# Kernel optimization log

Measured on AMD Instinct MI355X. Metric: run time of the kernel, lower is better.

Reference implementation:

```python
import jax, jax.numpy as jnp
import numpy as np

BN_EPS = 1e-5

def conv1x1(x, w, b):
    # x: [B,C,H,W], w: [O,C], b: [O]
    return jnp.einsum('bchw,oc->bohw', x, w) + b[None, :, None, None]

def bn_inf(x, gamma, beta, mean, var):
    inv = gamma / jnp.sqrt(var + BN_EPS)
    return (x - mean[None, :, None, None]) * inv[None, :, None, None] + beta[None, :, None, None]

def setup_inputs() -> dict:
    key = jax.random.key(0)
    ks = jax.random.split(key, 24)
    B, Fg, Fl, Fi = 8, 256, 256, 64
    H = W = 64
    c8 = Fi // 8
    d = {}
    d['g'] = jax.random.normal(ks[0], (B, Fg, H, W), jnp.float32)
    d['x'] = jax.random.normal(ks[1], (B, Fl, H, W), jnp.float32)
    # W_g: conv1x1 + BN
    d['Wg_w'] = jax.random.normal(ks[2], (Fi, Fg), jnp.float32) * (1.0 / np.sqrt(Fg))
    d['Wg_b'] = jax.random.normal(ks[3], (Fi,), jnp.float32) * 0.02
    d['bng_gamma'] = jax.random.uniform(ks[4], (Fi,), jnp.float32, 0.5, 1.5)
    d['bng_beta'] = jax.random.normal(ks[5], (Fi,), jnp.float32) * 0.1
    d['bng_mean'] = jax.random.normal(ks[6], (Fi,), jnp.float32) * 0.1
    d['bng_var'] = jax.random.uniform(ks[7], (Fi,), jnp.float32, 0.5, 1.5)
    # W_x: conv1x1 + BN
    d['Wx_w'] = jax.random.normal(ks[8], (Fi, Fl), jnp.float32) * (1.0 / np.sqrt(Fl))
    d['Wx_b'] = jax.random.normal(ks[9], (Fi,), jnp.float32) * 0.02
    d['bnx_gamma'] = jax.random.uniform(ks[10], (Fi,), jnp.float32, 0.5, 1.5)
    d['bnx_beta'] = jax.random.normal(ks[11], (Fi,), jnp.float32) * 0.1
    d['bnx_mean'] = jax.random.normal(ks[12], (Fi,), jnp.float32) * 0.1
    d['bnx_var'] = jax.random.uniform(ks[13], (Fi,), jnp.float32, 0.5, 1.5)
    # psi: conv1x1 (Fi->1) + BN(1) + sigmoid
    d['psi_w'] = jax.random.normal(ks[14], (1, Fi), jnp.float32) * (1.0 / np.sqrt(Fi))
    d['psi_b'] = jax.random.normal(ks[15], (1,), jnp.float32) * 0.02
    d['bnp_gamma'] = jax.random.uniform(ks[16], (1,), jnp.float32, 0.5, 1.5)
    d['bnp_beta'] = jax.random.normal(ks[17], (1,), jnp.float32) * 0.1
    d['bnp_mean'] = jax.random.normal(ks[18], (1,), jnp.float32) * 0.1
    d['bnp_var'] = jax.random.uniform(ks[19], (1,), jnp.float32, 0.5, 1.5)
    # PAM convs
    d['pb_w'] = jax.random.normal(ks[20], (c8, Fi), jnp.float32) * (1.0 / np.sqrt(Fi))
    d['pb_b'] = jnp.zeros((c8,), jnp.float32)
    d['pc_w'] = jax.random.normal(ks[21], (c8, Fi), jnp.float32) * (1.0 / np.sqrt(Fi))
    d['pc_b'] = jnp.zeros((c8,), jnp.float32)
    d['pd_w'] = jax.random.normal(ks[22], (Fi, Fi), jnp.float32) * (1.0 / np.sqrt(Fi))
    d['pd_b'] = jnp.zeros((Fi,), jnp.float32)
    # scalar gates (torch inits to 0; use small nonzero to exercise the path)
    d['alpha'] = jax.random.normal(ks[23], (1,), jnp.float32) * 0.05
    d['cam_beta'] = jax.random.normal(jax.random.fold_in(key, 99), (1,), jnp.float32) * 0.05
    return d

def _cam(psi, cam_beta):
    B, C, H, W = psi.shape
    feat = psi.reshape(B, C, H * W)                       # [B,C,HW]
    att = jnp.einsum('bcn,bdn->bcd', feat, feat)          # [B,C,C]
    att_new = jnp.max(att, axis=-1, keepdims=True) - att  # max-subtract trick
    att = jax.nn.softmax(att_new, axis=-1)
    out = jnp.einsum('bcd,bdn->bcn', att, feat).reshape(B, C, H, W)
    return cam_beta[0] * out + psi

def _pam(psi, pb_w, pb_b, pc_w, pc_b, pd_w, pd_b, alpha):
    B, C, H, W = psi.shape
    HW = H * W
    fb = conv1x1(psi, pb_w, pb_b).reshape(B, -1, HW)      # [B,C/8,HW]
    fc = conv1x1(psi, pc_w, pc_b).reshape(B, -1, HW)      # [B,C/8,HW]
    energy = jnp.einsum('bki,bkj->bij', fb, fc)           # [B,HW,HW]
    att = jax.nn.softmax(energy, axis=-1)
    fd = conv1x1(psi, pd_w, pd_b).reshape(B, C, HW)       # [B,C,HW]
    out = jnp.einsum('bcj,bij->bci', fd, att).reshape(B, C, H, W)
    return alpha[0] * out + psi

def reference(g, x, Wg_w, Wg_b, bng_gamma, bng_beta, bng_mean, bng_var,
              Wx_w, Wx_b, bnx_gamma, bnx_beta, bnx_mean, bnx_var,
              psi_w, psi_b, bnp_gamma, bnp_beta, bnp_mean, bnp_var,
              pb_w, pb_b, pc_w, pc_b, pd_w, pd_b, alpha, cam_beta):
    g1 = bn_inf(conv1x1(g, Wg_w, Wg_b), bng_gamma, bng_beta, bng_mean, bng_var)
    x1 = bn_inf(conv1x1(x, Wx_w, Wx_b), bnx_gamma, bnx_beta, bnx_mean, bnx_var)
    psi = jax.nn.relu(g1 + x1)                            # [B,F_int,H,W]
    cam = _cam(psi, cam_beta)
    pam = _pam(psi, pb_w, pb_b, pc_w, pc_b, pd_w, pd_b, alpha)
    gate = bn_inf(conv1x1(cam * pam, psi_w, psi_b), bnp_gamma, bnp_beta, bnp_mean, bnp_var)
    da = jax.nn.sigmoid(gate)                             # [B,1,H,W]
    return x * da
```

## Files before the change

### kernel.cpp

```cpp
#include <hip/hip_runtime.h>
#include <hip/hip_bf16.h>
#include <math.h>

#define BB 8
#define CIN 256
#define FI 64
#define HW 4096
#define C8 8
#define EPS 1e-5f
#define LOG2E 1.4426950408889634f

typedef __attribute__((ext_vector_type(8))) short bf16x8;
typedef __attribute__((ext_vector_type(4))) float f32x4;
typedef unsigned short u16;

static __device__ __forceinline__ u16 f2b(float x) {
    unsigned u = __builtin_bit_cast(unsigned, x);
    return (u16)((u + 0x8000u) >> 16);
}
static __device__ __forceinline__ unsigned cvtpk(float a, float b) {
    unsigned r;
    asm("v_cvt_pk_bf16_f32 %0, %1, %2" : "=v"(r) : "v"(a), "v"(b));
    return r;
}
static __device__ __forceinline__ float b2f(u16 v) {
    return __builtin_bit_cast(float, ((unsigned)v) << 16);
}

__global__ __launch_bounds__(256) void k_prep(
    const float* __restrict__ Wg, const float* __restrict__ Wgb,
    const float* __restrict__ gg, const float* __restrict__ gbeta,
    const float* __restrict__ gm, const float* __restrict__ gv,
    const float* __restrict__ Wx, const float* __restrict__ Wxb,
    const float* __restrict__ xg, const float* __restrict__ xbeta,
    const float* __restrict__ xm, const float* __restrict__ xv,
    const float* __restrict__ pbw, const float* __restrict__ pbb,
    const float* __restrict__ pcw, const float* __restrict__ pcb,
    const float* __restrict__ pdw, const float* __restrict__ pdb,
    u16* __restrict__ Wp, float* __restrict__ Cp,
    u16* __restrict__ Wcat, float* __restrict__ bcat)
{
    const int gid = blockIdx.x * 256 + threadIdx.x;
    for (int idx = gid; idx < FI * 512; idx += 4096) {
        int o = idx >> 9, k = idx & 511;
        float s, w;
        if (k < 256) { s = gg[o] * rsqrtf(gv[o] + EPS); w = Wg[o * 256 + k]; }
        else         { s = xg[o] * rsqrtf(xv[o] + EPS); w = Wx[o * 256 + k - 256]; }
        Wp[idx] = f2b(w * s);
    }
    for (int idx = gid; idx < 80 * 64; idx += 4096) {
        int row = idx >> 6, col = idx & 63;
        float w;
        if (row < 8)       w = pbw[row * 64 + col] * LOG2E;
        else if (row < 16) w = pcw[(row - 8) * 64 + col];
        else               w = pdw[(row - 16) * 64 + col];
        Wcat[idx] = f2b(w);
    }
    if (blockIdx.x == 0) {
        int tid = threadIdx.x;
        if (tid < FI) {
            float ig = gg[tid] * rsqrtf(gv[tid] + EPS);
            float ix = xg[tid] * rsqrtf(xv[tid] + EPS);
            Cp[tid] = (Wgb[tid] - gm[tid]) * ig + gbeta[tid]
                    + (Wxb[tid] - xm[tid]) * ix + xbeta[tid];
        }
        if (tid >= 64 && tid < 144) {
            int r = tid - 64;
            float bv = (r < 8) ? pbb[r] * LOG2E : (r < 16 ? pcb[r - 8] : pdb[r - 16]);
            bcat[r] = bv;
        }
    }
}

__global__ __launch_bounds__(256) void k_psi(
    const float* __restrict__ g, const float* __restrict__ x,
    const u16* __restrict__ Wp, const float* __restrict__ Cp,
    const u16* __restrict__ Wcat, const float* __restrict__ bcat,
    u16* __restrict__ psiB, u16* __restrict__ psiLo,
    u16* __restrict__ fbcT, u16* __restrict__ fdB)
{
    const int tid  = threadIdx.x;
    const int lane = tid & 63;
    const int w    = tid >> 6;
    const int n    = lane & 15;
    const int quad = lane >> 4;
    const int b    = blockIdx.y;
    const int p0   = blockIdx.x * 64;

    __shared__ u16 InT[64][72];
    __shared__ u16 Tbc[64][16];

    f32x4 acc[4];
#pragma unroll
    for (int mt = 0; mt < 4; ++mt) acc[mt] = (f32x4){0.f, 0.f, 0.f, 0.f};

    for (int kc = 0; kc < 8; ++kc) {
        const float* src = (kc < 4) ? g : x;
        const int ch0 = (kc & 3) * 64;
        __syncthreads();
#pragma unroll
        for (int r = 0; r < 4; ++r) {
            int ch = (tid >> 4) + r * 16;
            int px = (tid & 15) * 4;
            float4 v = *(const float4*)&src[((size_t)b * CIN + ch0 + ch) * HW + p0 + px];
            InT[px][ch]     = f2b(v.x);
            InT[px + 1][ch] = f2b(v.y);
            InT[px + 2][ch] = f2b(v.z);
            InT[px + 3][ch] = f2b(v.w);
        }
        __syncthreads();
#pragma unroll
        for (int ks = 0; ks < 2; ++ks) {
            const int kglob = kc * 64 + ks * 32;
            bf16x8 bfrag = *(const bf16x8*)&InT[w * 16 + n][ks * 32 + quad * 8];
#pragma unroll
            for (int mt = 0; mt < 4; ++mt) {
                bf16x8 af = *(const bf16x8*)&Wp[(mt * 16 + n) * 512 + kglob + quad * 8];
                acc[mt] = __builtin_amdgcn_mfma_f32_16x16x32_bf16(
                              af, bfrag, acc[mt], 0, 0, 0);
            }
        }
    }

    float pv[4][4];
#pragma unroll
    for (int mt = 0; mt < 4; ++mt)
#pragma unroll
        for (int r = 0; r < 4; ++r) {
            int c = mt * 16 + quad * 4 + r;
            float v = acc[mt][r] + Cp[c];
            v = v > 0.f ? v : 0.f;
            pv[mt][r] = v;
            u16 hb = f2b(v);
            size_t idx = ((size_t)b * FI + c) * HW + p0 + w * 16 + n;
            psiB[idx]  = hb;
            psiLo[idx] = f2b(v - b2f(hb));
        }
    __syncthreads();
#pragma unroll
    for (int mt = 0; mt < 4; ++mt) {
        *(unsigned*)&InT[w * 16 + n][mt * 16 + quad * 4]     = cvtpk(pv[mt][0], pv[mt][1]);
        *(unsigned*)&InT[w * 16 + n][mt * 16 + quad * 4 + 2] = cvtpk(pv[mt][2], pv[mt][3]);
    }
    __syncthreads();

    f32x4 facc[5];
#pragma unroll
    for (int nt = 0; nt < 5; ++nt) facc[nt] = (f32x4){0.f, 0.f, 0.f, 0.f};
#pragma unroll
    for (int ks = 0; ks < 2; ++ks) {
        bf16x8 af = *(const bf16x8*)&InT[w * 16 + n][ks * 32 + quad * 8];
#pragma unroll
        for (int nt = 0; nt < 5; ++nt) {
            bf16x8 bf = *(const bf16x8*)&Wcat[(nt * 16 + n) * FI + ks * 32 + quad * 8];
            facc[nt] = __builtin_amdgcn_mfma_f32_16x16x32_bf16(af, bf, facc[nt], 0, 0, 0);
        }
    }
    __syncthreads();

    {
        float bias = bcat[n];
#pragma unroll
        for (int r = 0; r < 4; ++r)
            Tbc[w * 16 + quad * 4 + r][n] = f2b(facc[0][r] + bias);
    }
#pragma unroll
    for (int nt = 1; nt < 5; ++nt) {
        int ch = (nt - 1) * 16 + n;
        float bias = bcat[nt * 16 + n];
        *(unsigned*)&InT[ch][w * 16 + quad * 4]     = cvtpk(facc[nt][0] + bias, facc[nt][1] + bias);
        *(unsigned*)&InT[ch][w * 16 + quad * 4 + 2] = cvtpk(facc[nt][2] + bias, facc[nt][3] + bias);
    }
    __syncthreads();
    {
        int row = tid >> 2, part = tid & 3;
        uint2 v = *(const uint2*)&Tbc[row][part * 4];
        *(uint2*)&fbcT[((size_t)b * HW + p0 + row) * 16 + part * 4] = v;
    }
#pragma unroll
    for (int rep = 0; rep < 2; ++rep) {
        int t = rep * 256 + tid;
        int ch = t >> 3, seg = t & 7;
        bf16x8 v = *(const bf16x8*)&InT[ch][seg * 8];
        *(bf16x8*)&fdB[((size_t)b * FI + ch) * HW + p0 + seg * 8] = v;
    }
}

__global__ __launch_bounds__(256) void k_gram(
    const u16* __restrict__ psiB, const u16* __restrict__ psiLo,
    float* __restrict__ Gp)
{
    const int tid  = threadIdx.x;
    const int lane = tid & 63;
    const int w    = tid >> 6;
    const int n    = lane & 15;
    const int quad = lane >> 4;
    const int s    = blockIdx.x;
    const int b    = blockIdx.y;

    f32x4 acc[4];
#pragma unroll
    for (int nt = 0; nt < 4; ++nt) acc[nt] = (f32x4){0.f, 0.f, 0.f, 0.f};

    for (int ks = 0; ks < 4; ++ks) {
        const int k0 = s * 128 + ks * 32;
        const size_t ra = ((size_t)b * FI + w * 16 + n) * HW + k0 + quad * 8;
        bf16x8 ah = *(const bf16x8*)&psiB[ra];
        bf16x8 al = *(const bf16x8*)&psiLo[ra];
#pragma unroll
        for (int nt = 0; nt < 4; ++nt) {
            const size_t rb = ((size_t)b * FI + nt * 16 + n) * HW + k0 + quad * 8;
            bf16x8 bh = *(const bf16x8*)&psiB[rb];
            bf16x8 bl = *(const bf16x8*)&psiLo[rb];
            acc[nt] = __builtin_amdgcn_mfma_f32_16x16x32_bf16(ah, bh, acc[nt], 0, 0, 0);
            acc[nt] = __builtin_amdgcn_mfma_f32_16x16x32_bf16(ah, bl, acc[nt], 0, 0, 0);
            acc[nt] = __builtin_amdgcn_mfma_f32_16x16x32_bf16(al, bh, acc[nt], 0, 0, 0);
        }
    }
#pragma unroll
    for (int nt = 0; nt < 4; ++nt)
#pragma unroll
        for (int r = 0; r < 4; ++r) {
            int i = w * 16 + quad * 4 + r;
            Gp[(((size_t)s * 8 + b) * 64 + i) * 64 + nt * 16 + n] = acc[nt][r];
        }
}

__global__ __launch_bounds__(256) void k_camsm(
    const float* __restrict__ Gp, float* __restrict__ att)
{
    const int tid = threadIdx.x, d = tid & 63, ty = tid >> 6;
    const int b = blockIdx.x, grp = blockIdx.y;
#pragma unroll 1
    for (int rr = 0; rr < 4; ++rr) {
        int i = grp * 16 + ty * 4 + rr;
        float gsum = 0.f;
#pragma unroll 1
        for (int s = 0; s < 32; ++s) gsum += Gp[(((size_t)s * 8 + b) * 64 + i) * 64 + d];
        float M = gsum;
#pragma unroll
        for (int msk = 1; msk < 64; msk <<= 1) M = fmaxf(M, __shfl_xor(M, msk));
        float a = M - gsum;
        float m2 = a;
#pragma unroll
        for (int msk = 1; msk < 64; msk <<= 1) m2 = fmaxf(m2, __shfl_xor(m2, msk));
        float p = __expf(a - m2);
        float ssum = p;
#pragma unroll
        for (int msk = 1; msk < 64; msk <<= 1) ssum += __shfl_xor(ssum, msk);
        att[((size_t)b * 64 + i) * 64 + d] = p / ssum;
    }
}

__global__ __launch_bounds__(256) void k_pam(
    const u16* __restrict__ fbcT, const u16* __restrict__ fdB,
    u16* __restrict__ Opart, float* __restrict__ ml)
{
    const int tid  = threadIdx.x;
    const int lane = tid & 63;
    const int w    = tid >> 6;
    const int n    = lane & 15;
    const int quad = lane >> 4;
    const int b    = blockIdx.x;
    const int i0   = blockIdx.y * 64;
    const int p    = blockIdx.z;
    const int jstart = p * 32, jend = jstart + 32;

    __shared__ u16 Ks[2][68][8];
    __shared__ u16 Vs[2][64][64];
    __shared__ u16 Ps[4][16][64];

    if (tid < 16) {
        ((unsigned*)&Ks[0][64][0])[tid] = 0u;
        ((unsigned*)&Ks[1][64][0])[tid] = 0u;
    }

    bf16x8 qfrag = {};
    if (quad == 0)
        qfrag = *(const bf16x8*)&fbcT[((size_t)b * HW + i0 + w * 16 + n) * 16];

    const int kkey = tid >> 1, khalf = tid & 1;
    const int vch  = tid >> 3, vseg  = tid & 7;
    const int vslot = (vseg ^ (vch & 7)) << 3;
    const int pswz  = n & 7;

    const u16* kp = fbcT + ((size_t)b * HW + jstart * 64) * 16 + 8;
    const u16* vp = fdB + (size_t)b * FI * HW + jstart * 64;

    uint2 kreg = make_uint2(0u, 0u);
    bf16x8 vreg0, vreg1;
    if (tid < 128) kreg = *(const uint2*)(kp + (size_t)kkey * 16 + khalf * 4);
    vreg0 = *(const bf16x8*)(vp + (size_t)vch * HW + vseg * 8);
    vreg1 = *(const bf16x8*)(vp + (size_t)(32 + vch) * HW + vseg * 8);

    f32x4 oacc[4];
#pragma unroll
    for (int mt = 0; mt < 4; ++mt) oacc[mt] = (f32x4){0.f, 0.f, 0.f, 0.f};
    float m = -1e30f, l = 0.f;

    int cur = 0;
    for (int jc = jstart; jc < jend; ++jc) {
        if (tid < 128) *(uint2*)&Ks[cur][kkey][khalf * 4] = kreg;
        *(bf16x8*)&Vs[cur][vch][vslot]      = vreg0;
        *(bf16x8*)&Vs[cur][32 + vch][vslot] = vreg1;
        if (jc + 1 < jend) {
            kp += 64 * 16;
            vp += 64;
            if (tid < 128) kreg = *(const uint2*)(kp + (size_t)kkey * 16 + khalf * 4);
            vreg0 = *(const bf16x8*)(vp + (size_t)vch * HW + vseg * 8);
            vreg1 = *(const bf16x8*)(vp + (size_t)(32 + vch) * HW + vseg * 8);
        }
        __syncthreads();

        f32x4 s[4];
        __builtin_amdgcn_s_setprio(1);
#pragma unroll
        for (int mt = 0; mt < 4; ++mt) {
            bf16x8 af = *(const bf16x8*)&Ks[cur][mt * 16 + n + quad][0];
            s[mt] = __builtin_amdgcn_mfma_f32_16x16x32_bf16(
                        af, qfrag, (f32x4){0.f, 0.f, 0.f, 0.f}, 0, 0, 0);
        }
        __builtin_amdgcn_s_setprio(0);

        float cmax = -1e30f;
#pragma unroll
        for (int mt = 0; mt < 4; ++mt)
            cmax = fmaxf(cmax, fmaxf(fmaxf(s[mt][0], s[mt][1]),
                                     fmaxf(s[mt][2], s[mt][3])));
        cmax = fmaxf(cmax, __shfl_xor(cmax, 16));
        cmax = fmaxf(cmax, __shfl_xor(cmax, 32));

        if (__any(cmax > m + 8.f)) {
            float mnew  = fmaxf(m, cmax);
            float scale = __builtin_amdgcn_exp2f(m - mnew);
            l *= scale;
#pragma unroll
            for (int mt = 0; mt < 4; ++mt) {
                oacc[mt][0] *= scale; oacc[mt][1] *= scale;
                oacc[mt][2] *= scale; oacc[mt][3] *= scale;
            }
            m = mnew;
        }

        float psum = 0.f;
        unsigned pw[4][2];
#pragma unroll
        for (int mt = 0; mt < 4; ++mt) {
            float e0 = __builtin_amdgcn_exp2f(s[mt][0] - m);
            float e1 = __builtin_amdgcn_exp2f(s[mt][1] - m);
            float e2 = __builtin_amdgcn_exp2f(s[mt][2] - m);
            float e3 = __builtin_amdgcn_exp2f(s[mt][3] - m);
            psum += (e0 + e1) + (e2 + e3);
            pw[mt][0] = cvtpk(e0, e1);
            pw[mt][1] = cvtpk(e2, e3);
        }
        l += psum;

#pragma unroll
        for (int mt = 0; mt < 4; ++mt) {
            int so = (((mt * 2 + (quad >> 1)) ^ pswz) << 3) + ((quad & 1) << 2);
            *(uint2*)&Ps[w][n][so] = make_uint2(pw[mt][0], pw[mt][1]);
        }
        asm volatile("s_waitcnt lgkmcnt(0)" ::: "memory");
        __builtin_amdgcn_sched_barrier(0);

        __builtin_amdgcn_s_setprio(1);
#pragma unroll
        for (int k0 = 0; k0 < 2; ++k0) {
            bf16x8 pf = *(const bf16x8*)&Ps[w][n][((k0 * 4 + quad) ^ pswz) << 3];
#pragma unroll
            for (int mt = 0; mt < 4; ++mt) {
                bf16x8 vf = *(const bf16x8*)
                    &Vs[cur][mt * 16 + n][((k0 * 4 + quad) ^ pswz) << 3];
                oacc[mt] = __builtin_amdgcn_mfma_f32_16x16x32_bf16(
                               vf, pf, oacc[mt], 0, 0, 0);
            }
        }
        __builtin_amdgcn_s_setprio(0);
        cur ^= 1;
    }

    l += __shfl_xor(l, 16);
    l += __shfl_xor(l, 32);
    const float rl = 1.f / l;
#pragma unroll
    for (int mt = 0; mt < 4; ++mt)
#pragma unroll
        for (int r = 0; r < 4; ++r) {
            int c = mt * 16 + quad * 4 + r;
            Opart[(((size_t)p * 8 + b) * FI + c) * HW + i0 + w * 16 + n] =
                f2b(oacc[mt][r] * rl);
        }
    if (quad == 0)
        ((float2*)ml)[((size_t)p * 8 + b) * HW + i0 + w * 16 + n] = make_float2(m, l);
}

__global__ __launch_bounds__(256) void k_final(
    const u16* __restrict__ psiB, const u16* __restrict__ psiLo,
    const float* __restrict__ att,
    const u16* __restrict__ Opart, const float* __restrict__ ml,
    const float* __restrict__ x,
    const float* __restrict__ psiw, const float* __restrict__ psib,
    const float* __restrict__ pg, const float* __restrict__ pbeta,
    const float* __restrict__ pm, const float* __restrict__ pv,
    const float* __restrict__ alpha, const float* __restrict__ camb,
    float* __restrict__ out)
{
    const int tid = threadIdx.x, tx = tid & 63, ty = tid >> 6;
    const int b = blockIdx.y, p0 = blockIdx.x * 64;
    __shared__ float tp[64][65];
    __shared__ float A[64][64];
    __shared__ float Zp[4][64];

#pragma unroll
    for (int r = 0; r < 16; ++r) {
        int c = ty * 16 + r;
        size_t idx = ((size_t)b * FI + c) * HW + p0 + tx;
        tp[c][tx] = b2f(psiB[idx]) + b2f(psiLo[idx]);
        A[c][tx]  = att[((size_t)b * 64 + c) * 64 + tx];
    }
    __syncthreads();

    float2 ml0 = ((const float2*)ml)[((size_t)0 * 8 + b) * HW + p0 + tx];
    float2 ml1 = ((const float2*)ml)[((size_t)1 * 8 + b) * HW + p0 + tx];
    float M  = fmaxf(ml0.x, ml1.x);
    float w0 = ml0.y * __builtin_amdgcn_exp2f(ml0.x - M);
    float w1 = ml1.y * __builtin_amdgcn_exp2f(ml1.x - M);
    float winv = 1.f / (w0 + w1);
    w0 *= winv; w1 *= winv;

    const float al = alpha[0], cb = camb[0];
    const int c0 = __builtin_amdgcn_readfirstlane(ty * 16);
    float acc[16];
#pragma unroll
    for (int i = 0; i < 16; ++i) acc[i] = 0.f;
#pragma unroll 16
    for (int d = 0; d < 64; ++d) {
        float v = tp[d][tx];
#pragma unroll
        for (int i = 0; i < 16; ++i) acc[i] += A[c0 + i][d] * v;
    }
    float z = 0.f;
#pragma unroll
    for (int i = 0; i < 16; ++i) {
        int c = c0 + i;
        float ps  = tp[c][tx];
        float cam = cb * acc[i] + ps;
        float oa = w0 * b2f(Opart[(((size_t)0 * 8 + b) * FI + c) * HW + p0 + tx])
                 + w1 * b2f(Opart[(((size_t)1 * 8 + b) * FI + c) * HW + p0 + tx]);
        float pam = al * oa + ps;
        z += psiw[c] * (cam * pam);
    }
    Zp[ty][tx] = z;
    __syncthreads();
    float zt = Zp[0][tx] + Zp[1][tx] + Zp[2][tx] + Zp[3][tx] + psib[0];
    float inv = pg[0] * rsqrtf(pv[0] + EPS);
    float gate = (zt - pm[0]) * inv + pbeta[0];
    float da = 1.f / (1.f + __expf(-gate));

#pragma unroll 8
    for (int r = 0; r < 64; ++r) {
        int cl = ty + 4 * r;
        size_t idx = ((size_t)b * CIN + cl) * HW + p0 + tx;
        out[idx] = x[idx] * da;
    }
}

extern "C" void kernel_launch(void* const* d_in, const int* in_sizes, int n_in,
                              void* d_out, int out_size, void* d_ws, size_t ws_size,
                              hipStream_t stream)
{
    const float* g     = (const float*)d_in[0];
    const float* x     = (const float*)d_in[1];
    const float* Wg_w  = (const float*)d_in[2];
    const float* Wg_b  = (const float*)d_in[3];
    const float* bng_g = (const float*)d_in[4];
    const float* bng_b = (const float*)d_in[5];
    const float* bng_m = (const float*)d_in[6];
    const float* bng_v = (const float*)d_in[7];
    const float* Wx_w  = (const float*)d_in[8];
    const float* Wx_b  = (const float*)d_in[9];
    const float* bnx_g = (const float*)d_in[10];
    const float* bnx_b = (const float*)d_in[11];
    const float* bnx_m = (const float*)d_in[12];
    const float* bnx_v = (const float*)d_in[13];
    const float* psi_w = (const float*)d_in[14];
    const float* psi_b = (const float*)d_in[15];
    const float* bnp_g = (const float*)d_in[16];
    const float* bnp_b = (const float*)d_in[17];
    const float* bnp_m = (const float*)d_in[18];
    const float* bnp_v = (const float*)d_in[19];
    const float* pb_w  = (const float*)d_in[20];
    const float* pb_b  = (const float*)d_in[21];
    const float* pc_w  = (const float*)d_in[22];
    const float* pc_b  = (const float*)d_in[23];
    const float* pd_w  = (const float*)d_in[24];
    const float* pd_b  = (const float*)d_in[25];
    const float* alpha = (const float*)d_in[26];
    const float* camb  = (const float*)d_in[27];
    float* out = (float*)d_out;

    float* ws   = (float*)d_ws;
    u16*  psiB  = (u16*)(ws);
    u16*  psiLo = (u16*)(ws + 1048576);
    u16*  fbcT  = (u16*)(ws + 2097152);
    u16*  fdB   = (u16*)(ws + 2359296);
    float* att  = ws + 3407872;
    u16*  Wp    = (u16*)(ws + 3440640);
    float* Cp   = ws + 3457024;
    u16*  Wcat  = (u16*)(ws + 3457088);
    float* bcat = ws + 3459648;
    float* mlws = ws + 3459744;
    float* Gp   = ws + 3590816;
    u16*  Opart = (u16*)(ws + 3590816);

    k_prep<<<dim3(16), 256, 0, stream>>>(Wg_w, Wg_b, bng_g, bng_b, bng_m, bng_v,
                                         Wx_w, Wx_b, bnx_g, bnx_b, bnx_m, bnx_v,
                                         pb_w, pb_b, pc_w, pc_b, pd_w, pd_b,
                                         Wp, Cp, Wcat, bcat);
    k_psi<<<dim3(64, 8), 256, 0, stream>>>(g, x, Wp, Cp, Wcat, bcat,
                                           psiB, psiLo, fbcT, fdB);
    k_gram<<<dim3(32, 8), 256, 0, stream>>>(psiB, psiLo, Gp);
    k_camsm<<<dim3(8, 4), 256, 0, stream>>>(Gp, att);
    k_pam<<<dim3(8, 64, 2), 256, 0, stream>>>(fbcT, fdB, Opart, mlws);
    k_final<<<dim3(64, 8), 256, 0, stream>>>(psiB, psiLo, att, Opart, mlws, x,
                                             psi_w, psi_b, bnp_g, bnp_b, bnp_m, bnp_v,
                                             alpha, camb, out);
}
```

Measured before the change: 290.2 us.

## Use MFMA for CAM matmul in final kernel and widen gram/softmax grids

The CAM attention-times-psi product in k_final moves from a scalar FMA loop over fp32 LDS tiles to bf16 MFMA. Attention is stored as bf16 and psi as split hi/lo bf16 in XOR-swizzled LDS, and the epilogue is rearranged to match the MFMA output layout with shuffle reductions. k_gram gains a z-dimension that splits output columns so more blocks run, and k_camsm is parallelised to one row per block with a cross-wave partial sum. This trades some attention precision (bf16 att) for fewer scalar FLOPs and better occupancy in small kernels.

```diff
diff --git a/kernel.cpp b/kernel.cpp
--- a/kernel.cpp
+++ b/kernel.cpp
@@ -197,10 +197,11 @@
     const int quad = lane >> 4;
     const int s    = blockIdx.x;
     const int b    = blockIdx.y;
-
-    f32x4 acc[4];
-#pragma unroll
-    for (int nt = 0; nt < 4; ++nt) acc[nt] = (f32x4){0.f, 0.f, 0.f, 0.f};
+    const int zz   = blockIdx.z;
+
+    f32x4 acc[2];
+#pragma unroll
+    for (int nt = 0; nt < 2; ++nt) acc[nt] = (f32x4){0.f, 0.f, 0.f, 0.f};
 
     for (int ks = 0; ks < 4; ++ks) {
         const int k0 = s * 128 + ks * 32;
@@ -208,8 +209,8 @@
         bf16x8 ah = *(const bf16x8*)&psiB[ra];
         bf16x8 al = *(const bf16x8*)&psiLo[ra];
 #pragma unroll
-        for (int nt = 0; nt < 4; ++nt) {
-            const size_t rb = ((size_t)b * FI + nt * 16 + n) * HW + k0 + quad * 8;
+        for (int nt = 0; nt < 2; ++nt) {
+            const size_t rb = ((size_t)b * FI + zz * 32 + nt * 16 + n) * HW + k0 + quad * 8;
             bf16x8 bh = *(const bf16x8*)&psiB[rb];
             bf16x8 bl = *(const bf16x8*)&psiLo[rb];
             acc[nt] = __builtin_amdgcn_mfma_f32_16x16x32_bf16(ah, bh, acc[nt], 0, 0, 0);
@@ -218,25 +219,31 @@
         }
     }
 #pragma unroll
-    for (int nt = 0; nt < 4; ++nt)
+    for (int nt = 0; nt < 2; ++nt)
 #pragma unroll
         for (int r = 0; r < 4; ++r) {
             int i = w * 16 + quad * 4 + r;
-            Gp[(((size_t)s * 8 + b) * 64 + i) * 64 + nt * 16 + n] = acc[nt][r];
+            Gp[(((size_t)s * 8 + b) * 64 + i) * 64 + zz * 32 + nt * 16 + n] = acc[nt][r];
         }
 }
 
 __global__ __launch_bounds__(256) void k_camsm(
     const float* __restrict__ Gp, float* __restrict__ att)
 {
-    const int tid = threadIdx.x, d = tid & 63, ty = tid >> 6;
-    const int b = blockIdx.x, grp = blockIdx.y;
-#pragma unroll 1
-    for (int rr = 0; rr < 4; ++rr) {
-        int i = grp * 16 + ty * 4 + rr;
-        float gsum = 0.f;
-#pragma unroll 1
-        for (int s = 0; s < 32; ++s) gsum += Gp[(((size_t)s * 8 + b) * 64 + i) * 64 + d];
+    const int tid = threadIdx.x, tx = tid & 63, ty = tid >> 6;
+    const int b = blockIdx.x, i = blockIdx.y;
+    __shared__ float part[4][64];
+
+    float gs = 0.f;
+#pragma unroll
+    for (int j = 0; j < 8; ++j) {
+        int s = ty * 8 + j;
+        gs += Gp[(((size_t)s * 8 + b) * 64 + i) * 64 + tx];
+    }
+    part[ty][tx] = gs;
+    __syncthreads();
+    if (tid < 64) {
+        float gsum = part[0][tx] + part[1][tx] + part[2][tx] + part[3][tx];
         float M = gsum;
 #pragma unroll
         for (int msk = 1; msk < 64; msk <<= 1) M = fmaxf(M, __shfl_xor(M, msk));
@@ -248,7 +255,7 @@
         float ssum = p;
 #pragma unroll
         for (int msk = 1; msk < 64; msk <<= 1) ssum += __shfl_xor(ssum, msk);
-        att[((size_t)b * 64 + i) * 64 + d] = p / ssum;
+        att[((size_t)b * 64 + i) * 64 + tx] = p / ssum;
     }
 }
 
@@ -406,61 +413,119 @@
     const float* __restrict__ alpha, const float* __restrict__ camb,
     float* __restrict__ out)
 {
-    const int tid = threadIdx.x, tx = tid & 63, ty = tid >> 6;
+    const int tid  = threadIdx.x;
+    const int lane = tid & 63;
+    const int w    = tid >> 6;
+    const int n    = lane & 15;
+    const int quad = lane >> 4;
     const int b = blockIdx.y, p0 = blockIdx.x * 64;
-    __shared__ float tp[64][65];
-    __shared__ float A[64][64];
+
+    __shared__ u16 Abf[64][64];
+    __shared__ u16 tpB[64][64];
+    __shared__ u16 tpLo[64][64];
+    __shared__ float Wc0[64], Wc1[64], Pw[64], daL[64];
     __shared__ float Zp[4][64];
 
-#pragma unroll
-    for (int r = 0; r < 16; ++r) {
-        int c = ty * 16 + r;
-        size_t idx = ((size_t)b * FI + c) * HW + p0 + tx;
-        tp[c][tx] = b2f(psiB[idx]) + b2f(psiLo[idx]);
-        A[c][tx]  = att[((size_t)b * 64 + c) * 64 + tx];
-    }
-    __syncthreads();
-
-    float2 ml0 = ((const float2*)ml)[((size_t)0 * 8 + b) * HW + p0 + tx];
-    float2 ml1 = ((const float2*)ml)[((size_t)1 * 8 + b) * HW + p0 + tx];
-    float M  = fmaxf(ml0.x, ml1.x);
-    float w0 = ml0.y * __builtin_amdgcn_exp2f(ml0.x - M);
-    float w1 = ml1.y * __builtin_amdgcn_exp2f(ml1.x - M);
-    float winv = 1.f / (w0 + w1);
-    w0 *= winv; w1 *= winv;
+    {
+        int c = tid >> 2, seg = tid & 3;
+        const float* ap = &att[((size_t)b * 64 + c) * 64 + seg * 16];
+        float4 v0 = *(const float4*)(ap);
+        float4 v1 = *(const float4*)(ap + 4);
+        float4 v2 = *(const float4*)(ap + 8);
+        float4 v3 = *(const float4*)(ap + 12);
+        float vv[16] = {v0.x, v0.y, v0.z, v0.w, v1.x, v1.y, v1.z, v1.w,
+                        v2.x, v2.y, v2.z, v2.w, v3.x, v3.y, v3.z, v3.w};
+#pragma unroll
+        for (int j = 0; j < 8; ++j) {
+            int d0 = seg * 16 + j * 2;
+            int phys = (((d0 >> 3) ^ (c & 7)) << 3) | (d0 & 7);
+            *(unsigned*)&Abf[c][phys] = cvtpk(vv[2 * j], vv[2 * j + 1]);
+        }
+    }
+    {
+        int px = tid & 63, grp = tid >> 6;
+#pragma unroll
+        for (int cc = 0; cc < 16; cc += 2) {
+            int c = grp * 16 + cc;
+            size_t i0 = ((size_t)b * FI + c) * HW + p0 + px;
+            unsigned hb = ((unsigned)psiB[i0]) | (((unsigned)psiB[i0 + HW]) << 16);
+            unsigned lb = ((unsigned)psiLo[i0]) | (((unsigned)psiLo[i0 + HW]) << 16);
+            int phys = (((c >> 3) ^ (px & 7)) << 3) | (c & 7);
+            *(unsigned*)&tpB[px][phys]  = hb;
+            *(unsigned*)&tpLo[px][phys] = lb;
+        }
+    }
+    if (tid < 64) {
+        Pw[tid] = psiw[tid];
+        float2 ml0 = ((const float2*)ml)[((size_t)0 * 8 + b) * HW + p0 + tid];
+        float2 ml1 = ((const float2*)ml)[((size_t)1 * 8 + b) * HW + p0 + tid];
+        float M  = fmaxf(ml0.x, ml1.x);
+        float w0 = ml0.y * __builtin_amdgcn_exp2f(ml0.x - M);
+        float w1 = ml1.y * __builtin_amdgcn_exp2f(ml1.x - M);
+        float winv = 1.f / (w0 + w1);
+        Wc0[tid] = w0 * winv; Wc1[tid] = w1 * winv;
+    }
+    __syncthreads();
+
+    f32x4 acc[4];
+#pragma unroll
+    for (int nt = 0; nt < 4; ++nt) acc[nt] = (f32x4){0.f, 0.f, 0.f, 0.f};
+#pragma unroll
+    for (int ks = 0; ks < 2; ++ks) {
+        int arow = w * 16 + n;
+        bf16x8 af = *(const bf16x8*)&Abf[arow][((ks * 4 + quad) ^ (arow & 7)) << 3];
+#pragma unroll
+        for (int nt = 0; nt < 4; ++nt) {
+            int brow = nt * 16 + n;
+            int boff = ((ks * 4 + quad) ^ (brow & 7)) << 3;
+            bf16x8 bh = *(const bf16x8*)&tpB[brow][boff];
+            bf16x8 bl = *(const bf16x8*)&tpLo[brow][boff];
+            acc[nt] = __builtin_amdgcn_mfma_f32_16x16x32_bf16(af, bh, acc[nt], 0, 0, 0);
+            acc[nt] = __builtin_amdgcn_mfma_f32_16x16x32_bf16(af, bl, acc[nt], 0, 0, 0);
+        }
+    }
 
     const float al = alpha[0], cb = camb[0];
-    const int c0 = __builtin_amdgcn_readfirstlane(ty * 16);
-    float acc[16];
-#pragma unroll
-    for (int i = 0; i < 16; ++i) acc[i] = 0.f;
-#pragma unroll 16
-    for (int d = 0; d < 64; ++d) {
-        float v = tp[d][tx];
-#pragma unroll
-        for (int i = 0; i < 16; ++i) acc[i] += A[c0 + i][d] * v;
-    }
-    float z = 0.f;
-#pragma unroll
-    for (int i = 0; i < 16; ++i) {
-        int c = c0 + i;
-        float ps  = tp[c][tx];
-        float cam = cb * acc[i] + ps;
-        float oa = w0 * b2f(Opart[(((size_t)0 * 8 + b) * FI + c) * HW + p0 + tx])
-                 + w1 * b2f(Opart[(((size_t)1 * 8 + b) * FI + c) * HW + p0 + tx]);
-        float pam = al * oa + ps;
-        z += psiw[c] * (cam * pam);
-    }
-    Zp[ty][tx] = z;
-    __syncthreads();
-    float zt = Zp[0][tx] + Zp[1][tx] + Zp[2][tx] + Zp[3][tx] + psib[0];
-    float inv = pg[0] * rsqrtf(pv[0] + EPS);
-    float gate = (zt - pm[0]) * inv + pbeta[0];
-    float da = 1.f / (1.f + __expf(-gate));
-
+    float z[4] = {0.f, 0.f, 0.f, 0.f};
+#pragma unroll
+    for (int nt = 0; nt < 4; ++nt) {
+        int px = nt * 16 + n;
+        float w0 = Wc0[px], w1 = Wc1[px];
+#pragma unroll
+        for (int r = 0; r < 4; ++r) {
+            int c = w * 16 + quad * 4 + r;
+            int phys = (((c >> 3) ^ (px & 7)) << 3) | (c & 7);
+            float ps  = b2f(tpB[px][phys]) + b2f(tpLo[px][phys]);
+            float cam = cb * acc[nt][r] + ps;
+            float oa = w0 * b2f(Opart[(((size_t)0 * 8 + b) * FI + c) * HW + p0 + px])
+                     + w1 * b2f(Opart[(((size_t)1 * 8 + b) * FI + c) * HW + p0 + px]);
+            float pam = al * oa + ps;
+            z[nt] += Pw[c] * (cam * pam);
+        }
+    }
+#pragma unroll
+    for (int nt = 0; nt < 4; ++nt) {
+        z[nt] += __shfl_xor(z[nt], 16);
+        z[nt] += __shfl_xor(z[nt], 32);
+    }
+    if (quad == 0) {
+#pragma unroll
+        for (int nt = 0; nt < 4; ++nt) Zp[w][nt * 16 + n] = z[nt];
+    }
+    __syncthreads();
+    if (tid < 64) {
+        float zt = Zp[0][tid] + Zp[1][tid] + Zp[2][tid] + Zp[3][tid] + psib[0];
+        float inv = pg[0] * rsqrtf(pv[0] + EPS);
+        float gate = (zt - pm[0]) * inv + pbeta[0];
+        daL[tid] = 1.f / (1.f + __expf(-gate));
+    }
+    __syncthreads();
+
+    const int tx = lane;
+    const float da = daL[tx];
 #pragma unroll 8
     for (int r = 0; r < 64; ++r) {
-        int cl = ty + 4 * r;
+        int cl = w + 4 * r;
         size_t idx = ((size_t)b * CIN + cl) * HW + p0 + tx;
         out[idx] = x[idx] * da;
     }
@@ -520,8 +585,8 @@
                                          Wp, Cp, Wcat, bcat);
     k_psi<<<dim3(64, 8), 256, 0, stream>>>(g, x, Wp, Cp, Wcat, bcat,
                                            psiB, psiLo, fbcT, fdB);
-    k_gram<<<dim3(32, 8), 256, 0, stream>>>(psiB, psiLo, Gp);
-    k_camsm<<<dim3(8, 4), 256, 0, stream>>>(Gp, att);
+    k_gram<<<dim3(32, 8, 2), 256, 0, stream>>>(psiB, psiLo, Gp);
+    k_camsm<<<dim3(8, 64), 256, 0, stream>>>(Gp, att);
     k_pam<<<dim3(8, 64, 2), 256, 0, stream>>>(fbcT, fdB, Opart, mlws);
     k_final<<<dim3(64, 8), 256, 0, stream>>>(psiB, psiLo, att, Opart, mlws, x,
                                              psi_w, psi_b, bnp_g, bnp_b, bnp_m, bnp_v,
```

New measurement: 247.8 us. 14.6% less time.
